# Kernel optimization log

Hardware: AMD Instinct MI355X
Metric: run time of the kernel (lower is better)

## Reference

```python
import jax, jax.numpy as jnp
import numpy as np

N = 100000   # nodes
E = 250000   # edges per relation
R = 4        # relations (etypes)
H = 4        # heads
D = 32       # per-head dim = hid_size // n_heads
IN = 256
HID = 128    # H * D
OUT = 64
SLOPE = 0.2  # DGL GATConv leaky_relu negative_slope


def setup_inputs() -> dict:
    key = jax.random.key(0)
    ks = jax.random.split(key, 16)
    rn = lambda k, shp, s: jax.random.normal(k, shp, dtype=jnp.float32) * s
    return {
        "x": rn(ks[0], (N, IN), 1.0),
        "src": jax.random.randint(ks[1], (R, E), 0, N, dtype=jnp.int32),
        "dst": jax.random.randint(ks[2], (R, E), 0, N, dtype=jnp.int32),
        "W0": rn(ks[3], (R, IN, HID), IN ** -0.5),
        "al0": rn(ks[4], (R, H, D), D ** -0.5),
        "ar0": rn(ks[5], (R, H, D), D ** -0.5),
        "b0": jnp.zeros((R, HID), jnp.float32),
        "W1": rn(ks[6], (R, HID, HID), HID ** -0.5),
        "al1": rn(ks[7], (R, H, D), D ** -0.5),
        "ar1": rn(ks[8], (R, H, D), D ** -0.5),
        "b1": jnp.zeros((R, HID), jnp.float32),
        "W2": rn(ks[9], (R, HID, HID), HID ** -0.5),
        "al2": rn(ks[10], (R, H, D), D ** -0.5),
        "ar2": rn(ks[11], (R, H, D), D ** -0.5),
        "b2": jnp.zeros((R, HID), jnp.float32),
        "fcW": rn(ks[12], (HID, OUT), HID ** -0.5),
        "fcb": jnp.zeros((OUT,), jnp.float32),
    }


def hetero_gat_layer(h, src, dst, W, al, ar, b):
    """HeteroGraphConv({etype: GATConv}, aggregate='sum') for one layer.

    h: [N, F_in]; W: [R, F_in, HID]; al/ar: [R, H, D]; b: [R, HID];
    src/dst: [R, E] int edge lists per relation.  Returns [N, HID].
    """
    feat = jnp.einsum('nf,rfo->rno', h, W).reshape(R, N, H, D)
    el = jnp.einsum('rnhd,rhd->rnh', feat, al)  # [R, N, H]
    er = jnp.einsum('rnhd,rhd->rnh', feat, ar)  # [R, N, H]

    def per_rel(feat_r, el_r, er_r, s, d, b_r):
        e = jax.nn.leaky_relu(el_r[s] + er_r[d], SLOPE)  # [E, H]
        # edge softmax over incoming edges of each destination node
        emax = jax.lax.stop_gradient(jax.ops.segment_max(e, d, num_segments=N))
        ee = jnp.exp(e - emax[d])
        denom = jax.ops.segment_sum(ee, d, num_segments=N)  # [N, H]
        alpha = ee / jnp.maximum(denom[d], 1e-9)             # [E, H]
        msg = feat_r[s] * alpha[:, :, None]                  # [E, H, D]
        out = jax.ops.segment_sum(msg, d, num_segments=N)    # [N, H, D]
        return out + b_r.reshape(H, D)                       # GATConv bias

    outs = jax.vmap(per_rel)(feat, el, er, src, dst, b)      # [R, N, H, D]
    # HeteroGraphConv aggregate='sum' across relations, then flatten heads
    return outs.sum(0).reshape(N, H * D)


def reference(x, src, dst, W0, al0, ar0, b0, W1, al1, ar1, b1, W2, al2, ar2, b2, fcW, fcb):
    h = jax.nn.relu(hetero_gat_layer(x, src, dst, W0, al0, ar0, b0))  # dropout = identity (eval)
    h = jax.nn.relu(hetero_gat_layer(h, src, dst, W1, al1, ar1, b1))
    h = hetero_gat_layer(h, src, dst, W2, al2, ar2, b2)               # last layer: no relu
    return h @ fcW + fcb                                              # self.fc on predict_category
```

## Files before the change

kernel.cpp:

```cpp
#include <hip/hip_runtime.h>
#include <hip/hip_bf16.h>

#define N_NODES 100000
#define N_EDGES 250000
#define N_REL 4
#define N_HEAD 4
#define D_HEAD 32
#define F_IN 256
#define F_HID 128
#define F_OUT 64
#define LRELU_SLOPE 0.2f

#define SCAN_B 256
#define NBLK ((N_NODES + SCAN_B - 1) / SCAN_B)

typedef __attribute__((ext_vector_type(8))) short s16x8;
typedef __attribute__((ext_vector_type(8))) unsigned short u16x8;
typedef __attribute__((ext_vector_type(4))) unsigned short u16x4;
typedef __attribute__((ext_vector_type(4))) float f32x4;

__device__ __forceinline__ float bf2f(unsigned short u) {
    return __uint_as_float(((unsigned int)u) << 16);
}
__device__ __forceinline__ unsigned short f2bf(float f) {
    unsigned int x = __float_as_uint(f);
    unsigned int r = x + 0x7fffu + ((x >> 16) & 1u);
    return (unsigned short)(r >> 16);
}
__device__ __forceinline__ void gload_lds16(const void* g, void* l) {
    __builtin_amdgcn_global_load_lds(
        (const __attribute__((address_space(1))) unsigned int*)g,
        (__attribute__((address_space(3))) unsigned int*)l, 16, 0, 0);
}

template<int FIN>
__global__ __launch_bounds__(256) void gemm_mfma_k(const unsigned short* __restrict__ A,
                                                   const unsigned short* __restrict__ BtAll,
                                                   unsigned short* __restrict__ CAll) {
    const int rel = blockIdx.x;
    const unsigned short* Bt = BtAll + (size_t)rel * F_HID * FIN;
    unsigned short* C = CAll + (size_t)rel * N_NODES * F_HID;

    __shared__ short As[128 * 64];
    __shared__ short Bs[128 * 64];
    const int tid = threadIdx.x;
    const int lane = tid & 63;
    const int wave = tid >> 6;
    const int wr = wave >> 1, wc = wave & 1;
    const int row0 = blockIdx.y * 128;

    f32x4 acc[4][4];
#pragma unroll
    for (int m = 0; m < 4; ++m)
#pragma unroll
        for (int n = 0; n < 4; ++n) acc[m][n] = (f32x4)0.f;

    for (int k0 = 0; k0 < FIN; k0 += 64) {
        if (k0) __syncthreads();
#pragma unroll
        for (int i = 0; i < 4; ++i) {
            int flat = i * 256 + tid;
            int r = flat >> 3, ch = flat & 7;
            int sch = ch ^ (r & 7);
            int grow = row0 + r; if (grow > N_NODES - 1) grow = N_NODES - 1;
            gload_lds16(A + (size_t)grow * FIN + k0 + sch * 8, As + (size_t)flat * 8);
        }
#pragma unroll
        for (int i = 0; i < 4; ++i) {
            int flat = i * 256 + tid;
            int r = flat >> 3, ch = flat & 7;
            int sch = ch ^ (r & 7);
            gload_lds16(Bt + (size_t)r * FIN + k0 + sch * 8, Bs + (size_t)flat * 8);
        }
        __syncthreads();
#pragma unroll
        for (int kk = 0; kk < 2; ++kk) {
            s16x8 a[4], b[4];
            const int kb = kk * 64 + (lane >> 4) * 16;
#pragma unroll
            for (int m = 0; m < 4; ++m) {
                int r = wr * 64 + m * 16 + (lane & 15);
                int off = r * 128 + (kb ^ ((r & 7) << 4));
                a[m] = *(const s16x8*)((const char*)As + off);
            }
#pragma unroll
            for (int n = 0; n < 4; ++n) {
                int r = wc * 64 + n * 16 + (lane & 15);
                int off = r * 128 + (kb ^ ((r & 7) << 4));
                b[n] = *(const s16x8*)((const char*)Bs + off);
            }
#pragma unroll
            for (int m = 0; m < 4; ++m)
#pragma unroll
                for (int n = 0; n < 4; ++n)
                    acc[m][n] = __builtin_amdgcn_mfma_f32_16x16x32_bf16(b[n], a[m], acc[m][n], 0, 0, 0);
        }
    }
#pragma unroll
    for (int m = 0; m < 4; ++m) {
        int r = row0 + wr * 64 + m * 16 + (lane & 15);
        if (r < N_NODES) {
#pragma unroll
            for (int n = 0; n < 4; ++n) {
                int cbase = wc * 64 + n * 16 + (lane >> 4) * 4;
                u16x4 o = {f2bf(acc[m][n][0]), f2bf(acc[m][n][1]),
                           f2bf(acc[m][n][2]), f2bf(acc[m][n][3])};
                *(u16x4*)(C + (size_t)r * F_HID + cbase) = o;
            }
        }
    }
}

template<int K>
__global__ __launch_bounds__(256) void wprep2_k(const float* __restrict__ W,
                                                const float* __restrict__ al,
                                                const float* __restrict__ ar,
                                                unsigned short* __restrict__ Wt,
                                                float* __restrict__ wal) {
    int i = blockIdx.x * 256 + threadIdx.x;
    if (i < N_REL * K * 128) {
        int r = i / (K * 128);
        int rem = i - r * K * 128;
        int k = rem >> 7, n = rem & 127;
        Wt[(size_t)r * 128 * K + (size_t)n * K + k] = f2bf(W[i]);
        return;
    }
    i -= N_REL * K * 128;
    if (i >= N_REL * K * 4) return;
    int rel = i / (K * 4);
    int rem = i - rel * K * 4;
    int f = rem >> 2, h = rem & 3;
    const float* wrow = W + ((size_t)rel * K + f) * F_HID + h * D_HEAD;
    const float* alv = al + ((size_t)rel * N_HEAD + h) * D_HEAD;
    const float* arv = ar + ((size_t)rel * N_HEAD + h) * D_HEAD;
    float sl = 0.f, sr = 0.f;
#pragma unroll
    for (int d = 0; d < D_HEAD; ++d) {
        float w = wrow[d];
        sl += w * alv[d];
        sr += w * arv[d];
    }
    wal[(size_t)f * 32 + rel * 4 + h] = sl;
    wal[(size_t)f * 32 + 16 + rel * 4 + h] = sr;
}

template<int FIN>
__global__ __launch_bounds__(256) void eler_wal_k(const unsigned short* __restrict__ hbf,
                                                  const float* __restrict__ wal,
                                                  float* __restrict__ el,
                                                  float* __restrict__ er) {
    __shared__ float walS[FIN * 32];
    for (int l = threadIdx.x; l < FIN * 8; l += 256)
        ((float4*)walS)[l] = ((const float4*)wal)[l];
    __syncthreads();
    const int jt = threadIdx.x & 3;
    const int rg = threadIdx.x >> 2;
    const int rbase = blockIdx.x * 256;
    float acc[4][8];
#pragma unroll
    for (int i = 0; i < 4; ++i)
#pragma unroll
        for (int o = 0; o < 8; ++o) acc[i][o] = 0.f;

    for (int f0 = 0; f0 < FIN; f0 += 8) {
        u16x8 hv8[4];
#pragma unroll
        for (int i = 0; i < 4; ++i) {
            int row = rbase + rg + 64 * i;
            hv8[i] = (row < N_NODES) ? *(const u16x8*)(hbf + (size_t)row * FIN + f0) : (u16x8)0;
        }
#pragma unroll
        for (int q = 0; q < 8; ++q) {
            float4 w0 = *(const float4*)&walS[(f0 + q) * 32 + jt * 8];
            float4 w1 = *(const float4*)&walS[(f0 + q) * 32 + jt * 8 + 4];
#pragma unroll
            for (int i = 0; i < 4; ++i) {
                float hv = bf2f(hv8[i][q]);
                acc[i][0] += hv * w0.x; acc[i][1] += hv * w0.y;
                acc[i][2] += hv * w0.z; acc[i][3] += hv * w0.w;
                acc[i][4] += hv * w1.x; acc[i][5] += hv * w1.y;
                acc[i][6] += hv * w1.z; acc[i][7] += hv * w1.w;
            }
        }
    }
#pragma unroll
    for (int i = 0; i < 4; ++i) {
        int row = rbase + rg + 64 * i;
        if (row < N_NODES) {
#pragma unroll
            for (int o = 0; o < 8; ++o) {
                int j = jt * 8 + o;
                int rel = (j >> 2) & 3, h = j & 3;
                float v = acc[i][o];
                if (j < 16) el[(size_t)rel * N_NODES * N_HEAD + row * 4 + h] = v;
                else        er[(size_t)rel * N_NODES * N_HEAD + row * 4 + h] = v;
            }
        }
    }
}

__global__ __launch_bounds__(256) void cast_k(const float* __restrict__ in,
                                              unsigned short* __restrict__ out, int n4) {
    int i = blockIdx.x * 256 + threadIdx.x;
    if (i >= n4) return;
    float4 v = *(const float4*)(in + (size_t)i * 4);
    u16x4 o = {f2bf(v.x), f2bf(v.y), f2bf(v.z), f2bf(v.w)};
    *(u16x4*)(out + (size_t)i * 4) = o;
}

__global__ __launch_bounds__(256) void count_k(const int* __restrict__ dst, int* __restrict__ cnt) {
    int e = blockIdx.x * 256 + threadIdx.x;
    if (e >= N_EDGES) return;
    int r = blockIdx.y;
    atomicAdd(&cnt[r * N_NODES + dst[(size_t)r * N_EDGES + e]], 1);
}

__global__ __launch_bounds__(SCAN_B) void scan1_k(const int* __restrict__ cnt,
                                                  int* __restrict__ row, int* __restrict__ bsum) {
    __shared__ int sdata[SCAN_B];
    int r = blockIdx.y;
    int n = blockIdx.x * SCAN_B + threadIdx.x;
    int v = (n < N_NODES) ? cnt[r * N_NODES + n] : 0;
    sdata[threadIdx.x] = v;
    __syncthreads();
    for (int off = 1; off < SCAN_B; off <<= 1) {
        int t = (threadIdx.x >= off) ? sdata[threadIdx.x - off] : 0;
        __syncthreads();
        sdata[threadIdx.x] += t;
        __syncthreads();
    }
    if (n < N_NODES) row[r * (N_NODES + 1) + n] = sdata[threadIdx.x] - v;
    if (threadIdx.x == SCAN_B - 1) bsum[r * NBLK + blockIdx.x] = sdata[threadIdx.x];
}

__global__ __launch_bounds__(512) void scan2_k(int* __restrict__ bsum) {
    __shared__ int sdata[512];
    int r = blockIdx.x;
    int v = (threadIdx.x < NBLK) ? bsum[r * NBLK + threadIdx.x] : 0;
    sdata[threadIdx.x] = v;
    __syncthreads();
    for (int off = 1; off < 512; off <<= 1) {
        int t = (threadIdx.x >= off) ? sdata[threadIdx.x - off] : 0;
        __syncthreads();
        sdata[threadIdx.x] += t;
        __syncthreads();
    }
    if (threadIdx.x < NBLK) bsum[r * NBLK + threadIdx.x] = sdata[threadIdx.x] - v;
}

__global__ __launch_bounds__(256) void scan3_k(int* __restrict__ row, const int* __restrict__ bsum) {
    int r = blockIdx.y;
    int n = blockIdx.x * 256 + threadIdx.x;
    if (n > N_NODES) return;
    if (n == N_NODES) { row[r * (N_NODES + 1) + N_NODES] = N_EDGES; return; }
    row[r * (N_NODES + 1) + n] += bsum[r * NBLK + n / SCAN_B];
}

__global__ __launch_bounds__(256) void fill_k(const int* __restrict__ src, const int* __restrict__ dst,
                                              const int* __restrict__ row, int* __restrict__ cursor,
                                              int* __restrict__ csr_src) {
    int e = blockIdx.x * 256 + threadIdx.x;
    if (e >= N_EDGES) return;
    int r = blockIdx.y;
    int s = src[(size_t)r * N_EDGES + e];
    int d = dst[(size_t)r * N_EDGES + e];
    int p = row[r * (N_NODES + 1) + d] + atomicAdd(&cursor[r * N_NODES + d], 1);
    csr_src[(size_t)r * N_EDGES + p] = s;
}

__global__ __launch_bounds__(256) void gather_fused_k(const int* __restrict__ csr_srcAll,
                                                      const int* __restrict__ rowAll,
                                                      const unsigned short* __restrict__ featAll,
                                                      const float* __restrict__ el,
                                                      const float* __restrict__ er,
                                                      const float* __restrict__ bias,
                                                      unsigned short* __restrict__ hbf,
                                                      int relu) {
    int j = blockIdx.x * 256 + threadIdx.x;
    if (j >= N_NODES * 16) return;
    int n = j >> 4, sub = j & 15;
    int h = sub >> 2;
    float acc[8];
#pragma unroll
    for (int q = 0; q < 8; ++q) acc[q] = 0.f;

#pragma unroll
    for (int rel = 0; rel < N_REL; ++rel) {
        const int* row = rowAll + (size_t)rel * (N_NODES + 1);
        const int* cs = csr_srcAll + (size_t)rel * N_EDGES;
        const float* elr = el + (size_t)rel * N_NODES * N_HEAD;
        const unsigned short* feat = featAll + (size_t)rel * N_NODES * F_HID;
        int st = row[n], en = row[n + 1];
        if (st == en) continue;
        float erd = er[(size_t)rel * N_NODES * N_HEAD + n * 4 + h];
        float sum = 0.f;
        float racc[8];
#pragma unroll
        for (int q = 0; q < 8; ++q) racc[q] = 0.f;
        for (int p = st; p < en; ++p) {
            int s = cs[p];
            float v = elr[s * 4 + h] + erd;
            v = v > 0.f ? v : LRELU_SLOPE * v;
            float ee = __expf(v);
            sum += ee;
            u16x8 f = *(const u16x8*)(feat + (size_t)s * F_HID + sub * 8);
#pragma unroll
            for (int q = 0; q < 8; ++q) racc[q] += ee * bf2f(f[q]);
        }
        float id = 1.f / fmaxf(sum, 1e-30f);
#pragma unroll
        for (int q = 0; q < 8; ++q) acc[q] += racc[q] * id;
    }

    int c0 = sub * 8;
    u16x8 o;
#pragma unroll
    for (int q = 0; q < 8; ++q) {
        int c = c0 + q;
        float bs = bias[c] + bias[128 + c] + bias[256 + c] + bias[384 + c];
        float t = acc[q] + bs;
        if (relu) t = fmaxf(t, 0.f);
        o[q] = f2bf(t);
    }
    *(u16x8*)(hbf + (size_t)n * F_HID + c0) = o;
}

__global__ __launch_bounds__(256) void fc_k(const unsigned short* __restrict__ Hm,
                                            const float* __restrict__ Wm,
                                            const float* __restrict__ bv,
                                            float* __restrict__ out) {
    __shared__ float Ws[F_HID][F_OUT];
    __shared__ float Hs[32][F_HID];
    const int tid = threadIdx.x;
    const int n0 = blockIdx.x * 32;
    const int tx = tid & 63, ty = tid >> 6;
#pragma unroll
    for (int l = 0; l < 8; ++l) {
        int flat = tid + l * 256;
        int r = flat >> 4, c4 = flat & 15;
        *(float4*)(&Ws[r][c4 * 4]) = *(const float4*)(Wm + r * F_OUT + c4 * 4);
    }
#pragma unroll
    for (int l = 0; l < 2; ++l) {
        int flat = tid + l * 256;
        int r = flat >> 4, c8 = flat & 15;
        u16x8 v = (u16x8)0;
        if (n0 + r < N_NODES)
            v = *(const u16x8*)(Hm + (size_t)(n0 + r) * F_HID + c8 * 8);
#pragma unroll
        for (int q = 0; q < 8; ++q) Hs[r][c8 * 8 + q] = bf2f(v[q]);
    }
    __syncthreads();
    float acc[8];
#pragma unroll
    for (int i = 0; i < 8; ++i) acc[i] = 0.f;
    for (int k = 0; k < F_HID; ++k) {
        float w = Ws[k][tx];
#pragma unroll
        for (int i = 0; i < 8; ++i) acc[i] += Hs[ty * 8 + i][k] * w;
    }
    float bb = bv[tx];
#pragma unroll
    for (int i = 0; i < 8; ++i) {
        int r = n0 + ty * 8 + i;
        if (r < N_NODES) out[(size_t)r * F_OUT + tx] = acc[i] + bb;
    }
}

extern "C" void kernel_launch(void* const* d_in, const int* in_sizes, int n_in,
                              void* d_out, int out_size, void* d_ws, size_t ws_size,
                              hipStream_t stream) {
    const float* x   = (const float*)d_in[0];
    const int*   src = (const int*)d_in[1];
    const int*   dst = (const int*)d_in[2];
    const float* W[3]  = {(const float*)d_in[3], (const float*)d_in[7],  (const float*)d_in[11]};
    const float* al[3] = {(const float*)d_in[4], (const float*)d_in[8],  (const float*)d_in[12]};
    const float* ar[3] = {(const float*)d_in[5], (const float*)d_in[9],  (const float*)d_in[13]};
    const float* bb[3] = {(const float*)d_in[6], (const float*)d_in[10], (const float*)d_in[14]};
    const float* fcW = (const float*)d_in[15];
    const float* fcb = (const float*)d_in[16];
    float* out = (float*)d_out;

    char* p = (char*)d_ws;
    unsigned short* hbf   = (unsigned short*)p; p += (size_t)N_NODES * F_IN * 2;
    unsigned short* featb = (unsigned short*)p; p += (size_t)N_REL * N_NODES * F_HID * 2;
    float* el    = (float*)p;               p += (size_t)N_REL * N_NODES * N_HEAD * 4;
    float* er    = (float*)p;               p += (size_t)N_REL * N_NODES * N_HEAD * 4;
    float* wal0  = (float*)p;               p += (size_t)F_IN * 32 * 4;
    float* wal1  = (float*)p;               p += (size_t)F_HID * 32 * 4;
    float* wal2  = (float*)p;               p += (size_t)F_HID * 32 * 4;
    unsigned short* Wt0   = (unsigned short*)p; p += (size_t)N_REL * F_IN * F_HID * 2;
    unsigned short* Wt1   = (unsigned short*)p; p += (size_t)N_REL * F_HID * F_HID * 2;
    unsigned short* Wt2   = (unsigned short*)p; p += (size_t)N_REL * F_HID * F_HID * 2;
    int* cnt     = (int*)p;                 p += (size_t)N_REL * N_NODES * 4;
    int* cursor  = (int*)p;                 p += (size_t)N_REL * N_NODES * 4;
    int* rowp    = (int*)p;                 p += (size_t)N_REL * (N_NODES + 1) * 4;
    int* bsum    = (int*)p;                 p += (size_t)N_REL * NBLK * 4;
    int* csr_src = (int*)p;                 p += (size_t)N_REL * N_EDGES * 4;

    const int eblk = (N_EDGES + 255) / 256;
    const dim3 egrid(eblk, N_REL);

    cast_k<<<(N_NODES * F_IN / 4 + 255) / 256, 256, 0, stream>>>(x, hbf, N_NODES * F_IN / 4);
    wprep2_k<F_IN><<<(N_REL * F_IN * 132 + 255) / 256, 256, 0, stream>>>(W[0], al[0], ar[0], Wt0, wal0);
    wprep2_k<F_HID><<<(N_REL * F_HID * 132 + 255) / 256, 256, 0, stream>>>(W[1], al[1], ar[1], Wt1, wal1);
    wprep2_k<F_HID><<<(N_REL * F_HID * 132 + 255) / 256, 256, 0, stream>>>(W[2], al[2], ar[2], Wt2, wal2);

    hipMemsetAsync(cnt, 0, 2 * (size_t)N_REL * N_NODES * sizeof(int), stream);
    count_k<<<egrid, 256, 0, stream>>>(dst, cnt);
    scan1_k<<<dim3(NBLK, N_REL), SCAN_B, 0, stream>>>(cnt, rowp, bsum);
    scan2_k<<<N_REL, 512, 0, stream>>>(bsum);
    scan3_k<<<dim3((N_NODES + 256) / 256, N_REL), 256, 0, stream>>>(rowp, bsum);
    fill_k<<<egrid, 256, 0, stream>>>(src, dst, rowp, cursor, csr_src);

    const dim3 gemm_grid(N_REL, (N_NODES + 127) / 128);
    const int ew_blocks = (N_NODES + 255) / 256;
    const int g_blocks  = (N_NODES * 16 + 255) / 256;
    const int fc_blocks = (N_NODES + 31) / 32;

    const unsigned short* Wts[3] = {Wt0, Wt1, Wt2};
    const float* wals[3] = {wal0, wal1, wal2};

    for (int layer = 0; layer < 3; ++layer) {
        if (layer == 0) {
            gemm_mfma_k<F_IN><<<gemm_grid, 256, 0, stream>>>(hbf, Wts[0], featb);
            eler_wal_k<F_IN><<<ew_blocks, 256, 0, stream>>>(hbf, wals[0], el, er);
        } else {
            gemm_mfma_k<F_HID><<<gemm_grid, 256, 0, stream>>>(hbf, Wts[layer], featb);
            eler_wal_k<F_HID><<<ew_blocks, 256, 0, stream>>>(hbf, wals[layer], el, er);
        }
        gather_fused_k<<<g_blocks, 256, 0, stream>>>(csr_src, rowp, featb, el, er,
                                                     bb[layer], hbf, layer < 2 ? 1 : 0);
    }
    fc_k<<<fc_blocks, 256, 0, stream>>>(hbf, fcW, fcb, out);
}
```

Measured before the change: 614.5 us.

## Fold el/er projection into MFMA GEMM as extra relation slice; unroll gather by two

The separate eler_wal kernel is removed. The folded attention weights (W·al, W·ar) are packed as a zero-padded 128-column bf16 B matrix, and the GEMM grid gains a fifth relation slot that computes el/er with MFMA and writes them straight out as float4. This saves one kernel launch and a second full read of the node features per layer, but it spends extra MFMA work on mostly zero columns and now rounds the folded weights to bf16. The gather loop is also unrolled by two edges so that feature and logit loads from independent sources can be in flight at the same time.

Result: faster. 521.0 us (-15.2%).

```diff
diff --git a/kernel.cpp b/kernel.cpp
--- a/kernel.cpp
+++ b/kernel.cpp
@@ -36,10 +36,12 @@
 template<int FIN>
 __global__ __launch_bounds__(256) void gemm_mfma_k(const unsigned short* __restrict__ A,
                                                    const unsigned short* __restrict__ BtAll,
-                                                   unsigned short* __restrict__ CAll) {
+                                                   const unsigned short* __restrict__ WalBt,
+                                                   unsigned short* __restrict__ CAll,
+                                                   float* __restrict__ el,
+                                                   float* __restrict__ er) {
     const int rel = blockIdx.x;
-    const unsigned short* Bt = BtAll + (size_t)rel * F_HID * FIN;
-    unsigned short* C = CAll + (size_t)rel * N_NODES * F_HID;
+    const unsigned short* Bt = (rel < N_REL) ? BtAll + (size_t)rel * F_HID * FIN : WalBt;
 
     __shared__ short As[128 * 64];
     __shared__ short Bs[128 * 64];
@@ -96,16 +98,29 @@
                     acc[m][n] = __builtin_amdgcn_mfma_f32_16x16x32_bf16(b[n], a[m], acc[m][n], 0, 0, 0);
         }
     }
-#pragma unroll
-    for (int m = 0; m < 4; ++m) {
-        int r = row0 + wr * 64 + m * 16 + (lane & 15);
-        if (r < N_NODES) {
-#pragma unroll
-            for (int n = 0; n < 4; ++n) {
-                int cbase = wc * 64 + n * 16 + (lane >> 4) * 4;
-                u16x4 o = {f2bf(acc[m][n][0]), f2bf(acc[m][n][1]),
-                           f2bf(acc[m][n][2]), f2bf(acc[m][n][3])};
-                *(u16x4*)(C + (size_t)r * F_HID + cbase) = o;
+    if (rel < N_REL) {
+        unsigned short* C = CAll + (size_t)rel * N_NODES * F_HID;
+#pragma unroll
+        for (int m = 0; m < 4; ++m) {
+            int r = row0 + wr * 64 + m * 16 + (lane & 15);
+            if (r < N_NODES) {
+#pragma unroll
+                for (int n = 0; n < 4; ++n) {
+                    int cbase = wc * 64 + n * 16 + (lane >> 4) * 4;
+                    u16x4 o = {f2bf(acc[m][n][0]), f2bf(acc[m][n][1]),
+                               f2bf(acc[m][n][2]), f2bf(acc[m][n][3])};
+                    *(u16x4*)(C + (size_t)r * F_HID + cbase) = o;
+                }
+            }
+        }
+    } else if (wc == 0) {
+        int relh = lane >> 4;
+#pragma unroll
+        for (int m = 0; m < 4; ++m) {
+            int r = row0 + wr * 64 + m * 16 + (lane & 15);
+            if (r < N_NODES) {
+                *(f32x4*)(el + (size_t)relh * N_NODES * N_HEAD + r * 4) = acc[m][0];
+                *(f32x4*)(er + (size_t)relh * N_NODES * N_HEAD + r * 4) = acc[m][1];
             }
         }
     }
@@ -116,87 +131,38 @@
                                                 const float* __restrict__ al,
                                                 const float* __restrict__ ar,
                                                 unsigned short* __restrict__ Wt,
-                                                float* __restrict__ wal) {
+                                                unsigned short* __restrict__ walbt) {
     int i = blockIdx.x * 256 + threadIdx.x;
-    if (i < N_REL * K * 128) {
+    const int nWt = N_REL * K * 128;
+    if (i < nWt) {
         int r = i / (K * 128);
         int rem = i - r * K * 128;
         int k = rem >> 7, n = rem & 127;
         Wt[(size_t)r * 128 * K + (size_t)n * K + k] = f2bf(W[i]);
         return;
     }
-    i -= N_REL * K * 128;
-    if (i >= N_REL * K * 4) return;
-    int rel = i / (K * 4);
-    int rem = i - rel * K * 4;
-    int f = rem >> 2, h = rem & 3;
-    const float* wrow = W + ((size_t)rel * K + f) * F_HID + h * D_HEAD;
-    const float* alv = al + ((size_t)rel * N_HEAD + h) * D_HEAD;
-    const float* arv = ar + ((size_t)rel * N_HEAD + h) * D_HEAD;
-    float sl = 0.f, sr = 0.f;
-#pragma unroll
-    for (int d = 0; d < D_HEAD; ++d) {
-        float w = wrow[d];
-        sl += w * alv[d];
-        sr += w * arv[d];
-    }
-    wal[(size_t)f * 32 + rel * 4 + h] = sl;
-    wal[(size_t)f * 32 + 16 + rel * 4 + h] = sr;
-}
-
-template<int FIN>
-__global__ __launch_bounds__(256) void eler_wal_k(const unsigned short* __restrict__ hbf,
-                                                  const float* __restrict__ wal,
-                                                  float* __restrict__ el,
-                                                  float* __restrict__ er) {
-    __shared__ float walS[FIN * 32];
-    for (int l = threadIdx.x; l < FIN * 8; l += 256)
-        ((float4*)walS)[l] = ((const float4*)wal)[l];
-    __syncthreads();
-    const int jt = threadIdx.x & 3;
-    const int rg = threadIdx.x >> 2;
-    const int rbase = blockIdx.x * 256;
-    float acc[4][8];
-#pragma unroll
-    for (int i = 0; i < 4; ++i)
-#pragma unroll
-        for (int o = 0; o < 8; ++o) acc[i][o] = 0.f;
-
-    for (int f0 = 0; f0 < FIN; f0 += 8) {
-        u16x8 hv8[4];
-#pragma unroll
-        for (int i = 0; i < 4; ++i) {
-            int row = rbase + rg + 64 * i;
-            hv8[i] = (row < N_NODES) ? *(const u16x8*)(hbf + (size_t)row * FIN + f0) : (u16x8)0;
-        }
-#pragma unroll
-        for (int q = 0; q < 8; ++q) {
-            float4 w0 = *(const float4*)&walS[(f0 + q) * 32 + jt * 8];
-            float4 w1 = *(const float4*)&walS[(f0 + q) * 32 + jt * 8 + 4];
-#pragma unroll
-            for (int i = 0; i < 4; ++i) {
-                float hv = bf2f(hv8[i][q]);
-                acc[i][0] += hv * w0.x; acc[i][1] += hv * w0.y;
-                acc[i][2] += hv * w0.z; acc[i][3] += hv * w0.w;
-                acc[i][4] += hv * w1.x; acc[i][5] += hv * w1.y;
-                acc[i][6] += hv * w1.z; acc[i][7] += hv * w1.w;
-            }
-        }
-    }
-#pragma unroll
-    for (int i = 0; i < 4; ++i) {
-        int row = rbase + rg + 64 * i;
-        if (row < N_NODES) {
-#pragma unroll
-            for (int o = 0; o < 8; ++o) {
-                int j = jt * 8 + o;
-                int rel = (j >> 2) & 3, h = j & 3;
-                float v = acc[i][o];
-                if (j < 16) el[(size_t)rel * N_NODES * N_HEAD + row * 4 + h] = v;
-                else        er[(size_t)rel * N_NODES * N_HEAD + row * 4 + h] = v;
-            }
-        }
-    }
+    i -= nWt;
+    const int nWal = N_REL * K * 4;
+    if (i < nWal) {
+        int rel = i / (K * 4);
+        int rem = i - rel * K * 4;
+        int f = rem >> 2, h = rem & 3;
+        const float* wrow = W + ((size_t)rel * K + f) * F_HID + h * D_HEAD;
+        const float* alv = al + ((size_t)rel * N_HEAD + h) * D_HEAD;
+        const float* arv = ar + ((size_t)rel * N_HEAD + h) * D_HEAD;
+        float sl = 0.f, sr = 0.f;
+#pragma unroll
+        for (int d = 0; d < D_HEAD; ++d) {
+            float w = wrow[d];
+            sl += w * alv[d];
+            sr += w * arv[d];
+        }
+        walbt[(size_t)(rel * 4 + h) * K + f] = f2bf(sl);
+        walbt[(size_t)(16 + rel * 4 + h) * K + f] = f2bf(sr);
+        return;
+    }
+    i -= nWal;
+    if (i < 96 * K) walbt[(size_t)32 * K + i] = 0;
 }
 
 __global__ __launch_bounds__(256) void cast_k(const float* __restrict__ in,
@@ -297,7 +263,24 @@
         float racc[8];
 #pragma unroll
         for (int q = 0; q < 8; ++q) racc[q] = 0.f;
-        for (int p = st; p < en; ++p) {
+        int p = st;
+        for (; p + 2 <= en; p += 2) {
+            int s0 = cs[p], s1 = cs[p + 1];
+            float e0 = elr[s0 * 4 + h];
+            float e1 = elr[s1 * 4 + h];
+            u16x8 f0 = *(const u16x8*)(feat + (size_t)s0 * F_HID + sub * 8);
+            u16x8 f1 = *(const u16x8*)(feat + (size_t)s1 * F_HID + sub * 8);
+            float v0 = e0 + erd; v0 = v0 > 0.f ? v0 : LRELU_SLOPE * v0;
+            float v1 = e1 + erd; v1 = v1 > 0.f ? v1 : LRELU_SLOPE * v1;
+            float ee0 = __expf(v0), ee1 = __expf(v1);
+            sum += ee0; sum += ee1;
+#pragma unroll
+            for (int q = 0; q < 8; ++q) {
+                racc[q] += ee0 * bf2f(f0[q]);
+                racc[q] += ee1 * bf2f(f1[q]);
+            }
+        }
+        if (p < en) {
             int s = cs[p];
             float v = elr[s * 4 + h] + erd;
             v = v > 0.f ? v : LRELU_SLOPE * v;
@@ -386,9 +369,9 @@
     unsigned short* featb = (unsigned short*)p; p += (size_t)N_REL * N_NODES * F_HID * 2;
     float* el    = (float*)p;               p += (size_t)N_REL * N_NODES * N_HEAD * 4;
     float* er    = (float*)p;               p += (size_t)N_REL * N_NODES * N_HEAD * 4;
-    float* wal0  = (float*)p;               p += (size_t)F_IN * 32 * 4;
-    float* wal1  = (float*)p;               p += (size_t)F_HID * 32 * 4;
-    float* wal2  = (float*)p;               p += (size_t)F_HID * 32 * 4;
+    unsigned short* walbt0 = (unsigned short*)p; p += (size_t)128 * F_IN * 2;
+    unsigned short* walbt1 = (unsigned short*)p; p += (size_t)128 * F_HID * 2;
+    unsigned short* walbt2 = (unsigned short*)p; p += (size_t)128 * F_HID * 2;
     unsigned short* Wt0   = (unsigned short*)p; p += (size_t)N_REL * F_IN * F_HID * 2;
     unsigned short* Wt1   = (unsigned short*)p; p += (size_t)N_REL * F_HID * F_HID * 2;
     unsigned short* Wt2   = (unsigned short*)p; p += (size_t)N_REL * F_HID * F_HID * 2;
@@ -402,9 +385,12 @@
     const dim3 egrid(eblk, N_REL);
 
     cast_k<<<(N_NODES * F_IN / 4 + 255) / 256, 256, 0, stream>>>(x, hbf, N_NODES * F_IN / 4);
-    wprep2_k<F_IN><<<(N_REL * F_IN * 132 + 255) / 256, 256, 0, stream>>>(W[0], al[0], ar[0], Wt0, wal0);
-    wprep2_k<F_HID><<<(N_REL * F_HID * 132 + 255) / 256, 256, 0, stream>>>(W[1], al[1], ar[1], Wt1, wal1);
-    wprep2_k<F_HID><<<(N_REL * F_HID * 132 + 255) / 256, 256, 0, stream>>>(W[2], al[2], ar[2], Wt2, wal2);
+    wprep2_k<F_IN><<<(N_REL * F_IN * 132 + 96 * F_IN + 255) / 256, 256, 0, stream>>>(
+        W[0], al[0], ar[0], Wt0, walbt0);
+    wprep2_k<F_HID><<<(N_REL * F_HID * 132 + 96 * F_HID + 255) / 256, 256, 0, stream>>>(
+        W[1], al[1], ar[1], Wt1, walbt1);
+    wprep2_k<F_HID><<<(N_REL * F_HID * 132 + 96 * F_HID + 255) / 256, 256, 0, stream>>>(
+        W[2], al[2], ar[2], Wt2, walbt2);
 
     hipMemsetAsync(cnt, 0, 2 * (size_t)N_REL * N_NODES * sizeof(int), stream);
     count_k<<<egrid, 256, 0, stream>>>(dst, cnt);
@@ -413,22 +399,20 @@
     scan3_k<<<dim3((N_NODES + 256) / 256, N_REL), 256, 0, stream>>>(rowp, bsum);
     fill_k<<<egrid, 256, 0, stream>>>(src, dst, rowp, cursor, csr_src);
 
-    const dim3 gemm_grid(N_REL, (N_NODES + 127) / 128);
-    const int ew_blocks = (N_NODES + 255) / 256;
+    const dim3 gemm_grid(N_REL + 1, (N_NODES + 127) / 128);
     const int g_blocks  = (N_NODES * 16 + 255) / 256;
     const int fc_blocks = (N_NODES + 31) / 32;
 
     const unsigned short* Wts[3] = {Wt0, Wt1, Wt2};
-    const float* wals[3] = {wal0, wal1, wal2};
+    const unsigned short* walbts[3] = {walbt0, walbt1, walbt2};
 
     for (int layer = 0; layer < 3; ++layer) {
-        if (layer == 0) {
-            gemm_mfma_k<F_IN><<<gemm_grid, 256, 0, stream>>>(hbf, Wts[0], featb);
-            eler_wal_k<F_IN><<<ew_blocks, 256, 0, stream>>>(hbf, wals[0], el, er);
-        } else {
-            gemm_mfma_k<F_HID><<<gemm_grid, 256, 0, stream>>>(hbf, Wts[layer], featb);
-            eler_wal_k<F_HID><<<ew_blocks, 256, 0, stream>>>(hbf, wals[layer], el, er);
-        }
+        if (layer == 0)
+            gemm_mfma_k<F_IN><<<gemm_grid, 256, 0, stream>>>(hbf, Wts[0], walbts[0],
+                                                             featb, el, er);
+        else
+            gemm_mfma_k<F_HID><<<gemm_grid, 256, 0, stream>>>(hbf, Wts[layer], walbts[layer],
+                                                              featb, el, er);
         gather_fused_k<<<g_blocks, 256, 0, stream>>>(csr_src, rowp, featb, el, er,
                                                      bb[layer], hbf, layer < 2 ? 1 : 0);
     }
```
